# Optimization experiments

Measured on AMD Instinct MI355X. Metric: run time of the kernel, lower is better.

## Reference

```python
import jax, jax.numpy as jnp
import numpy as np

D_MODEL = 1024
N_HEADS = 16
D_K = D_MODEL // N_HEADS


def setup_inputs() -> dict:
    key = jax.random.key(0)
    ks = jax.random.split(key, 12)
    B, P = 4, 1024
    s = 1.0 / np.sqrt(D_MODEL)
    inp = {
        'query': jax.random.normal(ks[0], (B, P, D_MODEL), jnp.float32),
        'key':   jax.random.normal(ks[1], (B, P, D_MODEL), jnp.float32),
        'value': jax.random.normal(ks[2], (B, P, D_MODEL), jnp.float32),
        'Wq': jax.random.normal(ks[3], (D_MODEL, D_MODEL), jnp.float32) * s,
        'bq': jnp.zeros((D_MODEL,), jnp.float32),
        'Wk': jax.random.normal(ks[4], (D_MODEL, D_MODEL), jnp.float32) * s,
        'bk': jnp.zeros((D_MODEL,), jnp.float32),
        'Wv': jax.random.normal(ks[5], (D_MODEL, D_MODEL), jnp.float32) * s,
        'bv': jnp.zeros((D_MODEL,), jnp.float32),
        'Wo': jax.random.normal(ks[6], (D_MODEL, D_MODEL), jnp.float32) * s,
        'bo': jnp.zeros((D_MODEL,), jnp.float32),
    }
    return inp


def reference(query, key, value, Wq, bq, Wk, bk, Wv, bv, Wo, bo):
    # Linear projections (torch Linear: x @ W.T + b)
    q = query @ Wq.T + bq
    k = key @ Wk.T + bk
    v = value @ Wv.T + bv
    B, P, _ = q.shape
    KP = k.shape[-2]
    # split heads: [B, H, P, d_k]
    q = q.reshape(B, P, N_HEADS, D_K).transpose(0, 2, 1, 3)
    k = k.reshape(B, KP, N_HEADS, D_K).transpose(0, 2, 1, 3)
    v = v.reshape(B, KP, N_HEADS, D_K).transpose(0, 2, 1, 3)
    # raw scores [B, H, P, KP]
    attn_score = jnp.einsum('bhpd,bhqd->bhpq', q, k) / jnp.sqrt(jnp.float32(D_K))
    # causal mask (masked=True path)
    causal = jnp.tril(jnp.ones((P, KP), bool))
    attn_score = jnp.where(causal, attn_score, -jnp.inf)
    probs = jax.nn.softmax(attn_score, axis=-1)
    out = jnp.einsum('bhpq,bhqd->bhpd', probs, v)
    out = out.transpose(0, 2, 1, 3).reshape(B, P, D_MODEL)
    out = out @ Wo.T + bo
    return out, attn_score
```

## Files before the change

kernel.cpp:

```cpp
#include <hip/hip_runtime.h>
#include <hip/hip_bf16.h>
#include <math.h>

#define D_MODEL 1024
#define NH 16
#define DK 64
#define BATCH 4
#define SEQ 1024
#define NEG_BIG (-1.0e30f)

typedef float f32x4 __attribute__((ext_vector_type(4)));
typedef short s16x8 __attribute__((ext_vector_type(8)));

__device__ __forceinline__ void gload_lds16(const void* g, void* l) {
    __builtin_amdgcn_global_load_lds((const __attribute__((address_space(1))) void*)g,
                                     (__attribute__((address_space(3))) void*)l, 16, 0, 0);
}

#define NW8 (D_MODEL * D_MODEL / 8)
#define NX8 (BATCH * SEQ * D_MODEL / 8)
__global__ __launch_bounds__(256) void cast_all(
        const float* __restrict__ Wq, const float* __restrict__ Wk,
        const float* __restrict__ Wv, const float* __restrict__ Wo,
        const float* __restrict__ q,  const float* __restrict__ k,
        const float* __restrict__ v,
        __hip_bfloat16* __restrict__ Wqb, __hip_bfloat16* __restrict__ Wkb,
        __hip_bfloat16* __restrict__ Wvb, __hip_bfloat16* __restrict__ Wob,
        __hip_bfloat16* __restrict__ Xq,  __hip_bfloat16* __restrict__ Xk,
        __hip_bfloat16* __restrict__ Xv) {
    int i = blockIdx.x * 256 + threadIdx.x;
    const float* src;
    __hip_bfloat16* dst;
    int o;
    if (i < 4 * NW8) {
        int seg = i >> 17; o = i & (NW8 - 1);
        src = seg == 0 ? Wq : seg == 1 ? Wk : seg == 2 ? Wv : Wo;
        dst = seg == 0 ? Wqb : seg == 1 ? Wkb : seg == 2 ? Wvb : Wob;
    } else {
        int j = i - 4 * NW8;
        int seg = j >> 19; o = j & (NX8 - 1);
        src = seg == 0 ? q : seg == 1 ? k : v;
        dst = seg == 0 ? Xq : seg == 1 ? Xk : Xv;
    }
    float4 x = ((const float4*)src)[2 * o];
    float4 y = ((const float4*)src)[2 * o + 1];
    alignas(16) __hip_bfloat16 ob[8];
    ob[0] = __float2bfloat16(x.x); ob[1] = __float2bfloat16(x.y);
    ob[2] = __float2bfloat16(x.z); ob[3] = __float2bfloat16(x.w);
    ob[4] = __float2bfloat16(y.x); ob[5] = __float2bfloat16(y.y);
    ob[6] = __float2bfloat16(y.z); ob[7] = __float2bfloat16(y.w);
    ((uint4*)dst)[o] = *(const uint4*)ob;
}

__device__ __forceinline__ void gemm_body(const __hip_bfloat16* __restrict__ A,
                                          const __hip_bfloat16* __restrict__ Bt,
                                          const float* __restrict__ bias,
                                          void* __restrict__ Cout, int mode) {
    __shared__ __align__(16) __hip_bfloat16 As[128 * 32];
    __shared__ __align__(16) __hip_bfloat16 Bs[128 * 32];
    const int K = D_MODEL, N = D_MODEL;
    const int t    = threadIdx.x;
    const int lane = t & 63;
    const int w    = t >> 6;
    const int wm   = (w >> 1) * 64;
    const int wn   = (w & 1) * 64;
    const int rl   = lane & 15;
    const int g    = lane >> 4;
    const int row0 = blockIdx.y * 128;
    const int col0 = blockIdx.x * 128;

    f32x4 acc[4][4] = {};

    for (int k0 = 0; k0 < K; k0 += 32) {
#pragma unroll
        for (int i = 0; i < 2; i++) {
            int c = w * 128 + i * 64 + lane;
            int r = c >> 2, ko = (c & 3) * 8;
            gload_lds16(A  + (size_t)(row0 + r) * K + k0 + ko,
                        As + (size_t)(w * 128 + i * 64) * 8);
            gload_lds16(Bt + (size_t)(col0 + r) * K + k0 + ko,
                        Bs + (size_t)(w * 128 + i * 64) * 8);
        }
        __syncthreads();
        s16x8 af[4], bf[4];
#pragma unroll
        for (int i = 0; i < 4; i++)
            af[i] = *(const s16x8*)&As[(wm + i * 16 + rl) * 32 + g * 8];
#pragma unroll
        for (int j = 0; j < 4; j++)
            bf[j] = *(const s16x8*)&Bs[(wn + j * 16 + rl) * 32 + g * 8];
#pragma unroll
        for (int i = 0; i < 4; i++)
#pragma unroll
            for (int j = 0; j < 4; j++)
                acc[i][j] = __builtin_amdgcn_mfma_f32_16x16x32_bf16(af[i], bf[j], acc[i][j], 0, 0, 0);
        __syncthreads();
    }

    if (mode == 0) {
        float* C = (float*)Cout;
#pragma unroll
        for (int j = 0; j < 4; j++) {
            int c = col0 + wn + j * 16 + rl;
            float bv = bias[c];
#pragma unroll
            for (int i = 0; i < 4; i++) {
                int rbase = row0 + wm + i * 16 + g * 4;
#pragma unroll
                for (int r = 0; r < 4; r++)
                    C[(size_t)(rbase + r) * N + c] = acc[i][j][r] + bv;
            }
        }
    } else if (mode == 1) {
        __hip_bfloat16* C = (__hip_bfloat16*)Cout;
#pragma unroll
        for (int j = 0; j < 4; j++) {
            int c = col0 + wn + j * 16 + rl;
            float bv = bias[c];
            int h = c >> 6, d = c & 63;
#pragma unroll
            for (int i = 0; i < 4; i++) {
                int rbase = row0 + wm + i * 16 + g * 4;
#pragma unroll
                for (int r = 0; r < 4; r++) {
                    int m = rbase + r;
                    int b = m >> 10, p = m & (SEQ - 1);
                    C[(((size_t)b * NH + h) * SEQ + p) * DK + d] =
                        __float2bfloat16(acc[i][j][r] + bv);
                }
            }
        }
    } else {
        __hip_bfloat16* C = (__hip_bfloat16*)Cout;
#pragma unroll
        for (int j = 0; j < 4; j++) {
            int c = col0 + wn + j * 16 + rl;
            float bv = bias[c];
            int h = c >> 6, d = c & 63;
#pragma unroll
            for (int i = 0; i < 4; i++) {
                int rbase = row0 + wm + i * 16 + g * 4;
                int b = rbase >> 10, p = rbase & (SEQ - 1);
                alignas(8) __hip_bfloat16 o4[4];
#pragma unroll
                for (int r = 0; r < 4; r++)
                    o4[r] = __float2bfloat16(acc[i][j][r] + bv);
                *(uint2*)&C[(((size_t)b * NH + h) * DK + d) * SEQ + p] = *(const uint2*)o4;
            }
        }
    }
}

__global__ __launch_bounds__(256) void gemm_bf16(const __hip_bfloat16* __restrict__ A,
                                                 const __hip_bfloat16* __restrict__ Bt,
                                                 const float* __restrict__ bias,
                                                 void* __restrict__ Cout, int mode) {
    gemm_body(A, Bt, bias, Cout, mode);
}

__global__ __launch_bounds__(256) void gemm_qkv(
        const __hip_bfloat16* __restrict__ Xq, const __hip_bfloat16* __restrict__ Xk,
        const __hip_bfloat16* __restrict__ Xv,
        const __hip_bfloat16* __restrict__ Wqb, const __hip_bfloat16* __restrict__ Wkb,
        const __hip_bfloat16* __restrict__ Wvb,
        const float* __restrict__ bq, const float* __restrict__ bk,
        const float* __restrict__ bv,
        __hip_bfloat16* __restrict__ qhm, __hip_bfloat16* __restrict__ khm,
        __hip_bfloat16* __restrict__ vtb) {
    if (blockIdx.z == 0)      gemm_body(Xq, Wqb, bq, qhm, 1);
    else if (blockIdx.z == 1) gemm_body(Xk, Wkb, bk, khm, 1);
    else                      gemm_body(Xv, Wvb, bv, vtb, 2);
}

__global__ __launch_bounds__(256) void scores_mfma(const __hip_bfloat16* __restrict__ qhm,
                                                   const __hip_bfloat16* __restrict__ khm,
                                                   float* __restrict__ S) {
    const int bh  = blockIdx.z;
    const int qi0 = blockIdx.y * 128;
    const int kj0 = blockIdx.x * 128;
    float* Sout = S + (size_t)bh * SEQ * SEQ;
    const int t = threadIdx.x;

    if (kj0 > qi0) {
        float4 neg = make_float4(NEG_BIG, NEG_BIG, NEG_BIG, NEG_BIG);
#pragma unroll
        for (int i = 0; i < 16; i++) {
            int idx = t + i * 256;
            int r = idx >> 5, c4 = idx & 31;
            *(float4*)&Sout[(size_t)(qi0 + r) * SEQ + kj0 + c4 * 4] = neg;
        }
        return;
    }

    __shared__ __align__(16) __hip_bfloat16 Qs[2 * 128 * 32];
    __shared__ __align__(16) __hip_bfloat16 Ks[2 * 128 * 32];
    const __hip_bfloat16* qb = qhm + (size_t)bh * SEQ * DK;
    const __hip_bfloat16* kb = khm + (size_t)bh * SEQ * DK;
    const int lane = t & 63;
    const int w    = t >> 6;
    const int rl   = lane & 15;
    const int g    = lane >> 4;
    const int wm   = (w >> 1) * 64;
    const int wn   = (w & 1) * 64;

#pragma unroll
    for (int i = 0; i < 4; i++) {
        int c  = w * 256 + i * 64 + lane;
        int r  = (c >> 2) & 127;
        int s  = c >> 9;
        int ko = (c & 3) * 8;
        gload_lds16(qb + (size_t)(qi0 + r) * DK + s * 32 + ko,
                    Qs + (size_t)(w * 256 + i * 64) * 8);
        gload_lds16(kb + (size_t)(kj0 + r) * DK + s * 32 + ko,
                    Ks + (size_t)(w * 256 + i * 64) * 8);
    }
    __syncthreads();

    f32x4 acc[4][4] = {};
#pragma unroll
    for (int s = 0; s < 2; s++) {
        s16x8 af[4], bf[4];
#pragma unroll
        for (int i = 0; i < 4; i++)
            af[i] = *(const s16x8*)&Qs[((s * 128) + wm + i * 16 + rl) * 32 + g * 8];
#pragma unroll
        for (int j = 0; j < 4; j++)
            bf[j] = *(const s16x8*)&Ks[((s * 128) + wn + j * 16 + rl) * 32 + g * 8];
#pragma unroll
        for (int i = 0; i < 4; i++)
#pragma unroll
            for (int j = 0; j < 4; j++)
                acc[i][j] = __builtin_amdgcn_mfma_f32_16x16x32_bf16(af[i], bf[j], acc[i][j], 0, 0, 0);
    }

    const float scale = 0.125f;
#pragma unroll
    for (int i = 0; i < 4; i++) {
        int qbase = qi0 + wm + i * 16 + g * 4;
#pragma unroll
        for (int j = 0; j < 4; j++) {
            int kj = kj0 + wn + j * 16 + rl;
#pragma unroll
            for (int r = 0; r < 4; r++) {
                int qi = qbase + r;
                Sout[(size_t)qi * SEQ + kj] = (kj <= qi) ? acc[i][j][r] * scale : NEG_BIG;
            }
        }
    }
}

__global__ __launch_bounds__(256) void pv_mfma(const float* __restrict__ S,
                                               const __hip_bfloat16* __restrict__ vt,
                                               __hip_bfloat16* __restrict__ ctx) {
    __shared__ __align__(16) __hip_bfloat16 Ps[128 * 136];
    __shared__ __align__(16) __hip_bfloat16 Vs[64 * 136];
    __shared__ float lrow[128];
    const int t  = threadIdx.x;
    const int bh = blockIdx.y;
    const int b  = bh >> 4;
    const int h  = bh & 15;
    const int p0 = blockIdx.x * 128;
    const float* Sb = S + (size_t)bh * SEQ * SEQ + (size_t)p0 * SEQ;
    const __hip_bfloat16* vb = vt + (size_t)bh * DK * SEQ;

    const int lane = t & 63;
    const int w    = t >> 6;
    const int rl   = lane & 15;
    const int g    = lane >> 4;
    const int wm   = (w >> 1) * 64;
    const int wn   = (w & 1) * 32;

    float lpart[16];
#pragma unroll
    for (int i = 0; i < 16; i++) lpart[i] = 0.f;

    f32x4 acc[4][2] = {};
    const int ntile = (p0 >> 7) + 1;
    for (int jt = 0; jt < ntile; jt++) {
        const int j0 = jt * 128;
#pragma unroll
        for (int it = 0; it < 16; it++) {
            int idx = it * 256 + t;
            int r = idx >> 5, c4 = idx & 31;
            float4 sv = *(const float4*)&Sb[(size_t)r * SEQ + j0 + c4 * 4];
            float px = __expf(sv.x), py = __expf(sv.y);
            float pz = __expf(sv.z), pw = __expf(sv.w);
            lpart[it] += (px + py) + (pz + pw);
            alignas(8) __hip_bfloat16 pb[4];
            pb[0] = __float2bfloat16(px);
            pb[1] = __float2bfloat16(py);
            pb[2] = __float2bfloat16(pz);
            pb[3] = __float2bfloat16(pw);
            *(uint2*)&Ps[r * 136 + c4 * 4] = *(const uint2*)pb;
        }
#pragma unroll
        for (int it = 0; it < 4; it++) {
            int idx = it * 256 + t;
            int r = idx >> 4, c = idx & 15;
            uint4 vv = *(const uint4*)&vb[(size_t)r * SEQ + j0 + c * 8];
            *(uint4*)&Vs[r * 136 + c * 8] = vv;
        }
        __syncthreads();
#pragma unroll
        for (int kk = 0; kk < 4; kk++) {
            s16x8 af[4], bf[2];
#pragma unroll
            for (int i = 0; i < 4; i++)
                af[i] = *(const s16x8*)&Ps[(wm + i * 16 + rl) * 136 + kk * 32 + g * 8];
#pragma unroll
            for (int j = 0; j < 2; j++)
                bf[j] = *(const s16x8*)&Vs[(wn + j * 16 + rl) * 136 + kk * 32 + g * 8];
#pragma unroll
            for (int i = 0; i < 4; i++)
#pragma unroll
                for (int j = 0; j < 2; j++)
                    acc[i][j] = __builtin_amdgcn_mfma_f32_16x16x32_bf16(af[i], bf[j], acc[i][j], 0, 0, 0);
        }
        __syncthreads();
    }

#pragma unroll
    for (int it = 0; it < 16; it++) {
        float s = lpart[it];
#pragma unroll
        for (int o = 16; o > 0; o >>= 1) s += __shfl_xor(s, o, 64);
        if ((t & 31) == 0) lrow[it * 8 + (t >> 5)] = s;
    }
    __syncthreads();

#pragma unroll
    for (int i = 0; i < 4; i++) {
#pragma unroll
        for (int r = 0; r < 4; r++) {
            int pl = wm + i * 16 + g * 4 + r;
            float il = 1.0f / lrow[pl];
            int p = p0 + pl;
#pragma unroll
            for (int j = 0; j < 2; j++) {
                int d = wn + j * 16 + rl;
                ctx[((size_t)(b * SEQ + p)) * D_MODEL + h * 64 + d] =
                    __float2bfloat16(acc[i][j][r] * il);
            }
        }
    }
}

extern "C" void kernel_launch(void* const* d_in, const int* in_sizes, int n_in,
                              void* d_out, int out_size, void* d_ws, size_t ws_size,
                              hipStream_t stream) {
    const float* query = (const float*)d_in[0];
    const float* key_  = (const float*)d_in[1];
    const float* value = (const float*)d_in[2];
    const float* Wq    = (const float*)d_in[3];
    const float* bq    = (const float*)d_in[4];
    const float* Wk    = (const float*)d_in[5];
    const float* bk    = (const float*)d_in[6];
    const float* Wv    = (const float*)d_in[7];
    const float* bv    = (const float*)d_in[8];
    const float* Wo    = (const float*)d_in[9];
    const float* bo    = (const float*)d_in[10];

    const size_t MB   = 1024 * 1024;
    const int    NTOK = BATCH * SEQ;
    char* wsb = (char*)d_ws;
    __hip_bfloat16* Xq  = (__hip_bfloat16*)wsb;
    __hip_bfloat16* Xk  = (__hip_bfloat16*)(wsb + 8  * MB);
    __hip_bfloat16* Xv  = (__hip_bfloat16*)(wsb + 16 * MB);
    __hip_bfloat16* Wqb = (__hip_bfloat16*)(wsb + 24 * MB);
    __hip_bfloat16* Wkb = (__hip_bfloat16*)(wsb + 26 * MB);
    __hip_bfloat16* Wvb = (__hip_bfloat16*)(wsb + 28 * MB);
    __hip_bfloat16* Wob = (__hip_bfloat16*)(wsb + 30 * MB);
    __hip_bfloat16* qhm = (__hip_bfloat16*)(wsb + 32 * MB);
    __hip_bfloat16* khm = (__hip_bfloat16*)(wsb + 40 * MB);
    __hip_bfloat16* Vtb = (__hip_bfloat16*)(wsb + 48 * MB);
    __hip_bfloat16* ctx = Xq;

    float* out    = (float*)d_out;
    float* scores = out + (size_t)NTOK * D_MODEL;

    cast_all<<<(4 * NW8 + 3 * NX8) / 256, 256, 0, stream>>>(
        Wq, Wk, Wv, Wo, query, key_, value,
        Wqb, Wkb, Wvb, Wob, Xq, Xk, Xv);

    dim3 pgrid(D_MODEL / 128, NTOK / 128);

    gemm_qkv<<<dim3(D_MODEL / 128, NTOK / 128, 3), 256, 0, stream>>>(
        Xq, Xk, Xv, Wqb, Wkb, Wvb, bq, bk, bv, qhm, khm, Vtb);

    scores_mfma<<<dim3(SEQ / 128, SEQ / 128, BATCH * NH), 256, 0, stream>>>(qhm, khm, scores);

    pv_mfma<<<dim3(SEQ / 128, BATCH * NH), 256, 0, stream>>>(scores, Vtb, ctx);

    gemm_bf16<<<pgrid, 256, 0, stream>>>(ctx, Wob, bo, out, 0);
}
```

Before: 490.7 us.

## Fuse score computation, softmax numerator and PV into one attention kernel

Merges the separate scores and PV kernels into one kernel per (query tile, head). It computes QK^T with MFMA in registers, writes the masked scores to the output, and exponentiates them straight into a swizzled LDS P tile for the PV MFMA. This drops the fp32 score read-back from global memory and one kernel launch, and adds an XOR swizzle on the LDS tiles to avoid bank conflicts. The cost is that the fully masked tiles are now written by the same blocks, which gives the causally imbalanced grid more serial work per block. Parallelism also drops to 512 blocks that each loop over K tiles.

Result: slower. 503.0 us (+2.5%).

```diff
diff --git a/kernel.cpp b/kernel.cpp
--- a/kernel.cpp
+++ b/kernel.cpp
@@ -172,160 +172,143 @@
     else                      gemm_body(Xv, Wvb, bv, vtb, 2);
 }
 
-__global__ __launch_bounds__(256) void scores_mfma(const __hip_bfloat16* __restrict__ qhm,
-                                                   const __hip_bfloat16* __restrict__ khm,
-                                                   float* __restrict__ S) {
-    const int bh  = blockIdx.z;
-    const int qi0 = blockIdx.y * 128;
-    const int kj0 = blockIdx.x * 128;
-    float* Sout = S + (size_t)bh * SEQ * SEQ;
-    const int t = threadIdx.x;
-
-    if (kj0 > qi0) {
-        float4 neg = make_float4(NEG_BIG, NEG_BIG, NEG_BIG, NEG_BIG);
-#pragma unroll
-        for (int i = 0; i < 16; i++) {
-            int idx = t + i * 256;
-            int r = idx >> 5, c4 = idx & 31;
-            *(float4*)&Sout[(size_t)(qi0 + r) * SEQ + kj0 + c4 * 4] = neg;
-        }
-        return;
-    }
-
-    __shared__ __align__(16) __hip_bfloat16 Qs[2 * 128 * 32];
-    __shared__ __align__(16) __hip_bfloat16 Ks[2 * 128 * 32];
-    const __hip_bfloat16* qb = qhm + (size_t)bh * SEQ * DK;
-    const __hip_bfloat16* kb = khm + (size_t)bh * SEQ * DK;
-    const int lane = t & 63;
-    const int w    = t >> 6;
-    const int rl   = lane & 15;
-    const int g    = lane >> 4;
-    const int wm   = (w >> 1) * 64;
-    const int wn   = (w & 1) * 64;
-
-#pragma unroll
-    for (int i = 0; i < 4; i++) {
-        int c  = w * 256 + i * 64 + lane;
-        int r  = (c >> 2) & 127;
-        int s  = c >> 9;
-        int ko = (c & 3) * 8;
-        gload_lds16(qb + (size_t)(qi0 + r) * DK + s * 32 + ko,
-                    Qs + (size_t)(w * 256 + i * 64) * 8);
-        gload_lds16(kb + (size_t)(kj0 + r) * DK + s * 32 + ko,
-                    Ks + (size_t)(w * 256 + i * 64) * 8);
-    }
-    __syncthreads();
-
-    f32x4 acc[4][4] = {};
-#pragma unroll
-    for (int s = 0; s < 2; s++) {
-        s16x8 af[4], bf[4];
-#pragma unroll
-        for (int i = 0; i < 4; i++)
-            af[i] = *(const s16x8*)&Qs[((s * 128) + wm + i * 16 + rl) * 32 + g * 8];
-#pragma unroll
-        for (int j = 0; j < 4; j++)
-            bf[j] = *(const s16x8*)&Ks[((s * 128) + wn + j * 16 + rl) * 32 + g * 8];
-#pragma unroll
-        for (int i = 0; i < 4; i++)
-#pragma unroll
-            for (int j = 0; j < 4; j++)
-                acc[i][j] = __builtin_amdgcn_mfma_f32_16x16x32_bf16(af[i], bf[j], acc[i][j], 0, 0, 0);
-    }
-
-    const float scale = 0.125f;
-#pragma unroll
-    for (int i = 0; i < 4; i++) {
-        int qbase = qi0 + wm + i * 16 + g * 4;
-#pragma unroll
-        for (int j = 0; j < 4; j++) {
-            int kj = kj0 + wn + j * 16 + rl;
-#pragma unroll
-            for (int r = 0; r < 4; r++) {
-                int qi = qbase + r;
-                Sout[(size_t)qi * SEQ + kj] = (kj <= qi) ? acc[i][j][r] * scale : NEG_BIG;
-            }
-        }
-    }
-}
-
-__global__ __launch_bounds__(256) void pv_mfma(const float* __restrict__ S,
-                                               const __hip_bfloat16* __restrict__ vt,
-                                               __hip_bfloat16* __restrict__ ctx) {
-    __shared__ __align__(16) __hip_bfloat16 Ps[128 * 136];
-    __shared__ __align__(16) __hip_bfloat16 Vs[64 * 136];
+__global__ __launch_bounds__(256) void attn_fused(const __hip_bfloat16* __restrict__ qhm,
+                                                  const __hip_bfloat16* __restrict__ khm,
+                                                  const __hip_bfloat16* __restrict__ vt,
+                                                  float* __restrict__ S,
+                                                  __hip_bfloat16* __restrict__ ctx) {
+    __shared__ __align__(16) char Psb[128 * 256];
+    __shared__ __align__(16) char Vsb[64 * 256];
+    __shared__ float lpartial[2][128];
     __shared__ float lrow[128];
     const int t  = threadIdx.x;
     const int bh = blockIdx.y;
     const int b  = bh >> 4;
     const int h  = bh & 15;
-    const int p0 = blockIdx.x * 128;
-    const float* Sb = S + (size_t)bh * SEQ * SEQ + (size_t)p0 * SEQ;
+    const int qt = blockIdx.x;
+    const int qi0 = qt * 128;
+    float* Sb = S + (size_t)bh * SEQ * SEQ;
+    const __hip_bfloat16* qb = qhm + (size_t)bh * SEQ * DK;
+    const __hip_bfloat16* kb = khm + (size_t)bh * SEQ * DK;
     const __hip_bfloat16* vb = vt + (size_t)bh * DK * SEQ;
 
     const int lane = t & 63;
     const int w    = t >> 6;
     const int rl   = lane & 15;
     const int g    = lane >> 4;
-    const int wm   = (w >> 1) * 64;
-    const int wn   = (w & 1) * 32;
-
-    float lpart[16];
-#pragma unroll
-    for (int i = 0; i < 16; i++) lpart[i] = 0.f;
-
+    const int qo  = (w & 1) * 64;
+    const int ko2 = (w >> 1) * 64;
+    const int wm = (w >> 1) * 64;
+    const int wn = (w & 1) * 32;
+    const int sw = (rl & 7) << 4;
+
+    s16x8 bfQ[2][4];
+#pragma unroll
+    for (int s = 0; s < 2; s++)
+#pragma unroll
+        for (int j = 0; j < 4; j++)
+            bfQ[s][j] = *(const s16x8*)&qb[(size_t)(qi0 + qo + j * 16 + rl) * DK + s * 32 + g * 8];
+
+    float lpart[4] = {0.f, 0.f, 0.f, 0.f};
     f32x4 acc[4][2] = {};
-    const int ntile = (p0 >> 7) + 1;
-    for (int jt = 0; jt < ntile; jt++) {
-        const int j0 = jt * 128;
-#pragma unroll
-        for (int it = 0; it < 16; it++) {
-            int idx = it * 256 + t;
-            int r = idx >> 5, c4 = idx & 31;
-            float4 sv = *(const float4*)&Sb[(size_t)r * SEQ + j0 + c4 * 4];
-            float px = __expf(sv.x), py = __expf(sv.y);
-            float pz = __expf(sv.z), pw = __expf(sv.w);
-            lpart[it] += (px + py) + (pz + pw);
-            alignas(8) __hip_bfloat16 pb[4];
-            pb[0] = __float2bfloat16(px);
-            pb[1] = __float2bfloat16(py);
-            pb[2] = __float2bfloat16(pz);
-            pb[3] = __float2bfloat16(pw);
-            *(uint2*)&Ps[r * 136 + c4 * 4] = *(const uint2*)pb;
-        }
+    const float scale = 0.125f;
+
+    for (int jt = 0; jt <= qt; jt++) {
+        const int kj0 = jt * 128;
+        s16x8 afK[2][4];
+#pragma unroll
+        for (int s = 0; s < 2; s++)
+#pragma unroll
+            for (int i = 0; i < 4; i++)
+                afK[s][i] = *(const s16x8*)&kb[(size_t)(kj0 + ko2 + i * 16 + rl) * DK + s * 32 + g * 8];
+        uint4 vr[4];
 #pragma unroll
         for (int it = 0; it < 4; it++) {
             int idx = it * 256 + t;
             int r = idx >> 4, c = idx & 15;
-            uint4 vv = *(const uint4*)&vb[(size_t)r * SEQ + j0 + c * 8];
-            *(uint4*)&Vs[r * 136 + c * 8] = vv;
+            vr[it] = *(const uint4*)&vb[(size_t)r * SEQ + kj0 + c * 8];
+        }
+        f32x4 s2[4][4] = {};
+#pragma unroll
+        for (int s = 0; s < 2; s++)
+#pragma unroll
+            for (int i = 0; i < 4; i++)
+#pragma unroll
+                for (int j = 0; j < 4; j++)
+                    s2[i][j] = __builtin_amdgcn_mfma_f32_16x16x32_bf16(afK[s][i], bfQ[s][j], s2[i][j], 0, 0, 0);
+#pragma unroll
+        for (int it = 0; it < 4; it++) {
+            int idx = it * 256 + t;
+            int r = idx >> 4, c = idx & 15;
+            *(uint4*)(Vsb + ((r * 256 + c * 16) ^ ((r & 7) << 4))) = vr[it];
+        }
+#pragma unroll
+        for (int i = 0; i < 4; i++) {
+            int kjb = kj0 + ko2 + i * 16 + g * 4;
+#pragma unroll
+            for (int j = 0; j < 4; j++) {
+                int qi = qi0 + qo + j * 16 + rl;
+                float4 sv;
+                float p4[4], sum = 0.f;
+#pragma unroll
+                for (int r = 0; r < 4; r++) {
+                    float sc = s2[i][j][r] * scale;
+                    bool ok = (kjb + r) <= qi;
+                    ((float*)&sv)[r] = ok ? sc : NEG_BIG;
+                    float pe = ok ? __expf(sc) : 0.f;
+                    p4[r] = pe;
+                    sum += pe;
+                }
+                *(float4*)&Sb[(size_t)qi * SEQ + kjb] = sv;
+                lpart[j] += sum;
+                alignas(8) __hip_bfloat16 pb[4];
+#pragma unroll
+                for (int r = 0; r < 4; r++) pb[r] = __float2bfloat16(p4[r]);
+                int qrow = qo + j * 16 + rl;
+                int kcol = ko2 + i * 16 + g * 4;
+                *(uint2*)(Psb + ((qrow * 256 + kcol * 2) ^ sw)) = *(const uint2*)pb;
+            }
         }
         __syncthreads();
 #pragma unroll
         for (int kk = 0; kk < 4; kk++) {
-            s16x8 af[4], bf[2];
+            s16x8 afP[4], bfV[2];
 #pragma unroll
             for (int i = 0; i < 4; i++)
-                af[i] = *(const s16x8*)&Ps[(wm + i * 16 + rl) * 136 + kk * 32 + g * 8];
+                afP[i] = *(const s16x8*)(Psb + (((wm + i * 16 + rl) * 256 + kk * 64 + g * 16) ^ sw));
 #pragma unroll
             for (int j = 0; j < 2; j++)
-                bf[j] = *(const s16x8*)&Vs[(wn + j * 16 + rl) * 136 + kk * 32 + g * 8];
+                bfV[j] = *(const s16x8*)(Vsb + (((wn + j * 16 + rl) * 256 + kk * 64 + g * 16) ^ sw));
 #pragma unroll
             for (int i = 0; i < 4; i++)
 #pragma unroll
                 for (int j = 0; j < 2; j++)
-                    acc[i][j] = __builtin_amdgcn_mfma_f32_16x16x32_bf16(af[i], bf[j], acc[i][j], 0, 0, 0);
+                    acc[i][j] = __builtin_amdgcn_mfma_f32_16x16x32_bf16(afP[i], bfV[j], acc[i][j], 0, 0, 0);
         }
         __syncthreads();
     }
 
-#pragma unroll
-    for (int it = 0; it < 16; it++) {
-        float s = lpart[it];
-#pragma unroll
-        for (int o = 16; o > 0; o >>= 1) s += __shfl_xor(s, o, 64);
-        if ((t & 31) == 0) lrow[it * 8 + (t >> 5)] = s;
-    }
+    {
+        float4 neg4 = make_float4(NEG_BIG, NEG_BIG, NEG_BIG, NEG_BIG);
+        for (int jt = qt + 1; jt < SEQ / 128; jt++) {
+#pragma unroll
+            for (int it = 0; it < 16; it++) {
+                int idx = it * 256 + t;
+                int r = idx >> 5, c4 = idx & 31;
+                *(float4*)&Sb[(size_t)(qi0 + r) * SEQ + jt * 128 + c4 * 4] = neg4;
+            }
+        }
+    }
+
+#pragma unroll
+    for (int j = 0; j < 4; j++) {
+        float v = lpart[j];
+        v += __shfl_xor(v, 16, 64);
+        v += __shfl_xor(v, 32, 64);
+        if (g == 0) lpartial[w >> 1][qo + j * 16 + rl] = v;
+    }
+    __syncthreads();
+    if (t < 128) lrow[t] = lpartial[0][t] + lpartial[1][t];
     __syncthreads();
 
 #pragma unroll
@@ -334,7 +317,7 @@
         for (int r = 0; r < 4; r++) {
             int pl = wm + i * 16 + g * 4 + r;
             float il = 1.0f / lrow[pl];
-            int p = p0 + pl;
+            int p = qi0 + pl;
 #pragma unroll
             for (int j = 0; j < 2; j++) {
                 int d = wn + j * 16 + rl;
@@ -387,9 +370,8 @@
     gemm_qkv<<<dim3(D_MODEL / 128, NTOK / 128, 3), 256, 0, stream>>>(
         Xq, Xk, Xv, Wqb, Wkb, Wvb, bq, bk, bv, qhm, khm, Vtb);
 
-    scores_mfma<<<dim3(SEQ / 128, SEQ / 128, BATCH * NH), 256, 0, stream>>>(qhm, khm, scores);
-
-    pv_mfma<<<dim3(SEQ / 128, BATCH * NH), 256, 0, stream>>>(scores, Vtb, ctx);
+    attn_fused<<<dim3(SEQ / 128, BATCH * NH), 256, 0, stream>>>(
+        qhm, khm, Vtb, scores, ctx);
 
     gemm_bf16<<<pgrid, 256, 0, stream>>>(ctx, Wob, bo, out, 0);
 }
```

## Balance causal PV work by pairing short and long 64-row query tiles per block

Applied to the files above, without the earlier changes.

The PV kernel now processes 64-row query tiles, and each block handles two of them: tile i and tile 15-i. Under causal masking this gives every block about the same number of key tiles and removes the tail imbalance where late-row blocks did far more work. The grid stays at 8x64 blocks, each doing two sequential passes with a smaller per-warp accumulator (2x2 MFMA tiles instead of 4x2). The trade-off is less MFMA work per LDS load and a tile granularity of 128 keys applied to 64-row tiles, so some masked exp work is redundant.

Measured after the change: 533.0 us. +8.6%, slower.

```diff
diff --git a/kernel.cpp b/kernel.cpp
--- a/kernel.cpp
+++ b/kernel.cpp
@@ -249,37 +249,32 @@
     }
 }
 
-__global__ __launch_bounds__(256) void pv_mfma(const float* __restrict__ S,
-                                               const __hip_bfloat16* __restrict__ vt,
-                                               __hip_bfloat16* __restrict__ ctx) {
-    __shared__ __align__(16) __hip_bfloat16 Ps[128 * 136];
+__device__ __forceinline__ void pv_body(const float* __restrict__ Sbh,
+                                        const __hip_bfloat16* __restrict__ vb,
+                                        __hip_bfloat16* __restrict__ ctx,
+                                        int b, int h, int q0) {
+    __shared__ __align__(16) __hip_bfloat16 Ps[64 * 136];
     __shared__ __align__(16) __hip_bfloat16 Vs[64 * 136];
-    __shared__ float lrow[128];
-    const int t  = threadIdx.x;
-    const int bh = blockIdx.y;
-    const int b  = bh >> 4;
-    const int h  = bh & 15;
-    const int p0 = blockIdx.x * 128;
-    const float* Sb = S + (size_t)bh * SEQ * SEQ + (size_t)p0 * SEQ;
-    const __hip_bfloat16* vb = vt + (size_t)bh * DK * SEQ;
-
+    __shared__ float lrow[64];
+    const int t    = threadIdx.x;
     const int lane = t & 63;
     const int w    = t >> 6;
     const int rl   = lane & 15;
     const int g    = lane >> 4;
-    const int wm   = (w >> 1) * 64;
-    const int wn   = (w & 1) * 32;
-
-    float lpart[16];
-#pragma unroll
-    for (int i = 0; i < 16; i++) lpart[i] = 0.f;
-
-    f32x4 acc[4][2] = {};
-    const int ntile = (p0 >> 7) + 1;
+    const int wq   = (w >> 1) * 32;
+    const int wd   = (w & 1) * 32;
+    const float* Sb = Sbh + (size_t)q0 * SEQ;
+
+    float lpart[8];
+#pragma unroll
+    for (int i = 0; i < 8; i++) lpart[i] = 0.f;
+    f32x4 acc[2][2] = {};
+
+    const int ntile = (q0 >> 7) + 1;
     for (int jt = 0; jt < ntile; jt++) {
         const int j0 = jt * 128;
 #pragma unroll
-        for (int it = 0; it < 16; it++) {
+        for (int it = 0; it < 8; it++) {
             int idx = it * 256 + t;
             int r = idx >> 5, c4 = idx & 31;
             float4 sv = *(const float4*)&Sb[(size_t)r * SEQ + j0 + c4 * 4];
@@ -297,30 +292,29 @@
         for (int it = 0; it < 4; it++) {
             int idx = it * 256 + t;
             int r = idx >> 4, c = idx & 15;
-            uint4 vv = *(const uint4*)&vb[(size_t)r * SEQ + j0 + c * 8];
-            *(uint4*)&Vs[r * 136 + c * 8] = vv;
+            *(uint4*)&Vs[r * 136 + c * 8] = *(const uint4*)&vb[(size_t)r * SEQ + j0 + c * 8];
         }
         __syncthreads();
 #pragma unroll
         for (int kk = 0; kk < 4; kk++) {
-            s16x8 af[4], bf[2];
-#pragma unroll
-            for (int i = 0; i < 4; i++)
-                af[i] = *(const s16x8*)&Ps[(wm + i * 16 + rl) * 136 + kk * 32 + g * 8];
+            s16x8 afP[2], bfV[2];
+#pragma unroll
+            for (int i = 0; i < 2; i++)
+                afP[i] = *(const s16x8*)&Ps[(wq + i * 16 + rl) * 136 + kk * 32 + g * 8];
 #pragma unroll
             for (int j = 0; j < 2; j++)
-                bf[j] = *(const s16x8*)&Vs[(wn + j * 16 + rl) * 136 + kk * 32 + g * 8];
-#pragma unroll
-            for (int i = 0; i < 4; i++)
+                bfV[j] = *(const s16x8*)&Vs[(wd + j * 16 + rl) * 136 + kk * 32 + g * 8];
+#pragma unroll
+            for (int i = 0; i < 2; i++)
 #pragma unroll
                 for (int j = 0; j < 2; j++)
-                    acc[i][j] = __builtin_amdgcn_mfma_f32_16x16x32_bf16(af[i], bf[j], acc[i][j], 0, 0, 0);
+                    acc[i][j] = __builtin_amdgcn_mfma_f32_16x16x32_bf16(afP[i], bfV[j], acc[i][j], 0, 0, 0);
         }
         __syncthreads();
     }
 
 #pragma unroll
-    for (int it = 0; it < 16; it++) {
+    for (int it = 0; it < 8; it++) {
         float s = lpart[it];
 #pragma unroll
         for (int o = 16; o > 0; o >>= 1) s += __shfl_xor(s, o, 64);
@@ -329,20 +323,35 @@
     __syncthreads();
 
 #pragma unroll
-    for (int i = 0; i < 4; i++) {
+    for (int i = 0; i < 2; i++) {
 #pragma unroll
         for (int r = 0; r < 4; r++) {
-            int pl = wm + i * 16 + g * 4 + r;
+            int pl = wq + i * 16 + g * 4 + r;
             float il = 1.0f / lrow[pl];
-            int p = p0 + pl;
+            int p = q0 + pl;
 #pragma unroll
             for (int j = 0; j < 2; j++) {
-                int d = wn + j * 16 + rl;
+                int d = wd + j * 16 + rl;
                 ctx[((size_t)(b * SEQ + p)) * D_MODEL + h * 64 + d] =
                     __float2bfloat16(acc[i][j][r] * il);
             }
         }
     }
+    __syncthreads();
+}
+
+__global__ __launch_bounds__(256) void pv_mfma(const float* __restrict__ S,
+                                               const __hip_bfloat16* __restrict__ vt,
+                                               __hip_bfloat16* __restrict__ ctx) {
+    const int bh = blockIdx.y;
+    const int b  = bh >> 4;
+    const int h  = bh & 15;
+    const float* Sbh = S + (size_t)bh * SEQ * SEQ;
+    const __hip_bfloat16* vb = vt + (size_t)bh * DK * SEQ;
+    const int qs1 = blockIdx.x;
+    const int qs2 = 15 - qs1;
+    pv_body(Sbh, vb, ctx, b, h, qs1 * 64);
+    pv_body(Sbh, vb, ctx, b, h, qs2 * 64);
 }
 
 extern "C" void kernel_launch(void* const* d_in, const int* in_sizes, int n_in,
@@ -389,7 +398,7 @@
 
     scores_mfma<<<dim3(SEQ / 128, SEQ / 128, BATCH * NH), 256, 0, stream>>>(qhm, khm, scores);
 
-    pv_mfma<<<dim3(SEQ / 128, BATCH * NH), 256, 0, stream>>>(scores, Vtb, ctx);
+    pv_mfma<<<dim3(8, BATCH * NH), 256, 0, stream>>>(scores, Vtb, ctx);
 
     gemm_bf16<<<pgrid, 256, 0, stream>>>(ctx, Wob, bo, out, 0);
 }
```
